# Kernel optimization log

Measured on AMD Instinct MI355X. Metric: run time of the kernel, lower is better.

The kernel has to match this reference:

```python
import jax, jax.numpy as jnp
import numpy as np

B, SEQ, D = 2, 1024, 768
E, H = 8, 3072          # num_experts, expert hidden (mlp_ratio=4)
CAPACITY = 2            # k = CAPACITY * num_tokens


def setup_inputs() -> dict:
    key = jax.random.key(0)
    ks = jax.random.split(key, 6)
    x = jax.random.normal(ks[0], (B, SEQ, D), dtype=jnp.float32)
    gate_weight = jax.random.normal(ks[1], (E, D), dtype=jnp.float32) * 0.006
    w1 = jax.random.normal(ks[2], (E, D, H), dtype=jnp.float32) * (1.0 / np.sqrt(D))
    b1 = jnp.zeros((E, H), dtype=jnp.float32)
    w2 = jax.random.normal(ks[3], (E, H, D), dtype=jnp.float32) * (1.0 / np.sqrt(H))
    b2 = jnp.zeros((E, D), dtype=jnp.float32)
    return {"x": x, "gate_weight": gate_weight, "w1": w1, "b1": b1, "w2": w2, "b2": b2}


def reference(x, gate_weight, w1, b1, w2, b2):
    Bb, s, d = x.shape
    xf = x.reshape(-1, d)                     # [S, D]
    S = xf.shape[0]
    k = S * CAPACITY
    logits = xf @ gate_weight.T               # [S, E]
    scores = jax.nn.softmax(logits, axis=-1).T  # [E, S]
    # flattened top-k over all (expert, token) pairs -> sparse gate matrix
    vals, idx = jax.lax.top_k(scores.reshape(-1), k)
    gate = jnp.zeros((E * S,), dtype=x.dtype).at[idx].add(vals).reshape(E, S)
    # expert MLPs (GELU-tanh) applied per expert; zero gate entries kill
    # non-routed (expert, token) pairs -> same math as gather/MLP/scatter.
    h = jax.nn.gelu(jnp.einsum('sd,edh->esh', xf, w1) + b1[:, None, :], approximate=True)
    out = jnp.einsum('esh,ehd->esd', h, w2) + b2[:, None, :]   # [E, S, D]
    y = jnp.einsum('es,esd->sd', gate, out)    # weighted combine + sum over experts
    return y.reshape(Bb, s, d)
```

## Files before the change

### kernel.cpp

```cpp
#include <hip/hip_runtime.h>
#include <math.h>

#define S_TOK 2048
#define NEXP  8
#define DDIM  768
#define HDIM  3072
#define KSEL  4096

typedef __attribute__((ext_vector_type(8))) short short8;
typedef __attribute__((ext_vector_type(4))) float f32x4;
typedef __attribute__((ext_vector_type(2))) unsigned int u32x2;

__device__ __forceinline__ unsigned short f2bf(float f) {
  unsigned u = __float_as_uint(f);
  u += 0x7fffu + ((u >> 16) & 1u);
  return (unsigned short)(u >> 16);
}

__device__ __forceinline__ float gelu_fast(float v) {
  float u = 0.7978845608028654f * (v + 0.044715f * v * v * v);
  float t = __expf(-2.0f * fabsf(u));
  float th = (1.0f - t) / (1.0f + t);
  th = copysignf(th, u);
  return 0.5f * v * (1.0f + th);
}

__global__ __launch_bounds__(256) void zero_kernel(float* __restrict__ p, int n) {
  int i = blockIdx.x * 256 + threadIdx.x;
  if (i < n) p[i] = 0.f;
}

__global__ __launch_bounds__(256) void convx_kernel(const float* __restrict__ x,
                                                    short* __restrict__ xb) {
  int i = (blockIdx.x * 256 + threadIdx.x) * 8;
  float4 a = *(const float4*)(x + i);
  float4 b = *(const float4*)(x + i + 4);
  short8 v;
  v[0] = (short)f2bf(a.x); v[1] = (short)f2bf(a.y);
  v[2] = (short)f2bf(a.z); v[3] = (short)f2bf(a.w);
  v[4] = (short)f2bf(b.x); v[5] = (short)f2bf(b.y);
  v[6] = (short)f2bf(b.z); v[7] = (short)f2bf(b.w);
  *(short8*)(xb + i) = v;
}

__global__ __launch_bounds__(256) void gate_kernel(
    const float* __restrict__ x, const float* __restrict__ gw,
    float* __restrict__ scores)
{
  int tid  = threadIdx.x;
  int lane = tid & 63;
  int wid  = tid >> 6;
  int token = blockIdx.x * 4 + wid;
  const float* xr = x + (size_t)token * DDIM;

  float acc[NEXP];
#pragma unroll
  for (int e = 0; e < NEXP; ++e) acc[e] = 0.f;

  for (int d = lane; d < DDIM; d += 64) {
    float xv = xr[d];
#pragma unroll
    for (int e = 0; e < NEXP; ++e) acc[e] += xv * gw[e * DDIM + d];
  }
#pragma unroll
  for (int e = 0; e < NEXP; ++e) {
    for (int off = 32; off; off >>= 1) acc[e] += __shfl_down(acc[e], off, 64);
  }
  if (lane == 0) {
    float m = acc[0];
#pragma unroll
    for (int e = 1; e < NEXP; ++e) m = fmaxf(m, acc[e]);
    float p[NEXP], s = 0.f;
#pragma unroll
    for (int e = 0; e < NEXP; ++e) { p[e] = expf(acc[e] - m); s += p[e]; }
    float inv = 1.0f / s;
#pragma unroll
    for (int e = 0; e < NEXP; ++e) scores[e * S_TOK + token] = p[e] * inv;
  }
}

__device__ unsigned block_scan_excl(unsigned v, volatile unsigned* wsum) {
  int tid = threadIdx.x, lane = tid & 63, wid = tid >> 6;
  __syncthreads();
  unsigned x = v;
#pragma unroll
  for (int off = 1; off < 64; off <<= 1) {
    unsigned t = __shfl_up(x, off, 64);
    if (lane >= off) x += t;
  }
  if (lane == 63) wsum[wid] = x;
  __syncthreads();
  if (tid < 64) {
    unsigned w = (lane < 16) ? wsum[lane] : 0u;
#pragma unroll
    for (int off = 1; off < 16; off <<= 1) {
      unsigned t = __shfl_up(w, off, 64);
      if (lane >= off) w += t;
    }
    if (lane < 16) wsum[lane] = w;
  }
  __syncthreads();
  unsigned woff = (wid > 0) ? wsum[wid - 1] : 0u;
  return woff + (x - v);
}

__global__ __launch_bounds__(1024) void select_kernel(
    const float* __restrict__ scores,
    int* __restrict__ tokenlist, float* __restrict__ slotgate,
    int* __restrict__ offsets)
{
  __shared__ unsigned cnt;
  __shared__ unsigned wsum[16];
  int tid = threadIdx.x;
  int base = tid * 16;

  float sv[16]; unsigned key[16];
#pragma unroll
  for (int j = 0; j < 16; ++j) {
    sv[j] = scores[base + j];
    key[j] = __float_as_uint(sv[j]);
  }

  unsigned lo = 0, hi = 0x3F800000u;
  while (lo < hi) {
    unsigned mid = lo + ((hi - lo + 1) >> 1);
    if (tid == 0) cnt = 0;
    __syncthreads();
    unsigned c = 0;
#pragma unroll
    for (int j = 0; j < 16; ++j) c += (key[j] >= mid) ? 1u : 0u;
    for (int off = 32; off; off >>= 1) c += __shfl_down(c, off, 64);
    if ((tid & 63) == 0) atomicAdd(&cnt, c);
    __syncthreads();
    unsigned tot = cnt;
    __syncthreads();
    if (tot >= (unsigned)KSEL) lo = mid; else hi = mid - 1;
  }
  unsigned V = lo;

  if (tid == 0) cnt = 0;
  __syncthreads();
  {
    unsigned c = 0;
#pragma unroll
    for (int j = 0; j < 16; ++j) c += (key[j] > V) ? 1u : 0u;
    for (int off = 32; off; off >>= 1) c += __shfl_down(c, off, 64);
    if ((tid & 63) == 0) atomicAdd(&cnt, c);
  }
  __syncthreads();
  int need = KSEL - (int)cnt;
  __syncthreads();

  unsigned tloc = 0;
#pragma unroll
  for (int j = 0; j < 16; ++j) tloc += (key[j] == V) ? 1u : 0u;
  unsigned texcl = block_scan_excl(tloc, wsum);

  unsigned selmask = 0, sloc = 0, trun = texcl;
#pragma unroll
  for (int j = 0; j < 16; ++j) {
    bool f;
    if (key[j] > V) f = true;
    else if (key[j] == V) { f = ((int)trun < need); ++trun; }
    else f = false;
    if (f) { selmask |= (1u << j); ++sloc; }
  }
  unsigned sexcl = block_scan_excl(sloc, wsum);

  if ((tid & 127) == 0) offsets[tid >> 7] = (int)sexcl;
  if (tid == 0) offsets[NEXP] = KSEL;

  unsigned p = sexcl;
#pragma unroll
  for (int j = 0; j < 16; ++j) {
    int i = base + j;
    if (selmask & (1u << j)) {
      tokenlist[p] = i & (S_TOK - 1);
      slotgate[p] = sv[j];
      ++p;
    }
  }
}

template <int MODE>
__global__ __launch_bounds__(256) void moe_mfma(
    const short* __restrict__ Abase, const float* __restrict__ W,
    const float* __restrict__ bias, void* __restrict__ outp,
    const int* __restrict__ offsets, const int* __restrict__ tokenlist,
    const float* __restrict__ slotgate)
{
  const int e = (int)blockIdx.x;
  const int K = (MODE == 1) ? DDIM : HDIM;
  const int N = (MODE == 1) ? HDIM : DDIM;
  const int tile  = (MODE == 1) ? (int)blockIdx.z : ((int)blockIdx.z >> 2);
  const int split = (MODE == 1) ? 0 : ((int)blockIdx.z & 3);
  const int klen  = 768;
  const int kb = split * klen;

  const int r0 = offsets[e];
  const int rows = offsets[e + 1] - r0;
  const int rowbase = tile << 7;
  if (rowbase >= rows) return;
  int vr = rows - rowbase; if (vr > 128) vr = 128;
  const int colbase = (int)blockIdx.y << 7;

  __shared__ short As0[128 * 40];
  __shared__ short As1[128 * 40];
  __shared__ __align__(16) short Bs0[32 * 128];
  __shared__ __align__(16) short Bs1[32 * 128];
  const unsigned bs0_lds = (unsigned)(uintptr_t)&Bs0[0];
  const unsigned bs1_lds = (unsigned)(uintptr_t)&Bs1[0];

  const int tid = threadIdx.x;
  const int lane = tid & 63;
  const int wid = tid >> 6;
  const int wr = (wid >> 1) << 6;
  const int wc = (wid & 1) << 6;
  const int l15 = lane & 15;
  const int lq = lane >> 4;

  const int ar = tid >> 1;
  const int ak = (tid & 1) << 4;
  const short* arow;
  {
    int cr = (ar < vr) ? ar : (vr - 1);
    if (MODE == 1) arow = Abase + (size_t)tokenlist[r0 + rowbase + cr] * DDIM;
    else           arow = Abase + (size_t)(r0 + rowbase + cr) * HDIM + kb;
  }

  const int sk = tid >> 3;
  const int g8 = tid & 7;
  const float* wsrc = W + (size_t)e * K * N + (size_t)kb * N + colbase + g8 * 16;
  const int bwoff = ((((sk >> 2) << 3) + g8) << 6) + ((sk & 3) << 4);

  f32x4 acc[4][4];
#pragma unroll
  for (int i = 0; i < 4; ++i)
#pragma unroll
    for (int j = 0; j < 4; ++j) acc[i][j] = (f32x4){0.f, 0.f, 0.f, 0.f};

  short8 avA0, avA1;
  float4 bw[4];

#define LOAD_AB(KN)                                              \
  {                                                              \
    avA0 = *(const short8*)(arow + (KN) + ak);                   \
    avA1 = *(const short8*)(arow + (KN) + ak + 8);               \
    const float* wp = wsrc + (size_t)((KN) + sk) * N;            \
    _Pragma("unroll")                                            \
    for (int q = 0; q < 4; ++q) bw[q] = *(const float4*)(wp + 4 * q); \
  }

#define WRITE_LDS(AS, BS)                                        \
  {                                                              \
    *(short8*)&AS[ar * 40 + ak] = avA0;                          \
    *(short8*)&AS[ar * 40 + ak + 8] = avA1;                      \
    _Pragma("unroll")                                            \
    for (int q = 0; q < 4; ++q) {                                \
      u32x2 pk;                                                  \
      pk[0] = (unsigned)f2bf(bw[q].x) | ((unsigned)f2bf(bw[q].y) << 16); \
      pk[1] = (unsigned)f2bf(bw[q].z) | ((unsigned)f2bf(bw[q].w) << 16); \
      *(u32x2*)((short*)BS + bwoff + 4 * q) = pk;                \
    }                                                            \
  }

#define KSTEP(RA, RBLDS, WA, WB, KC)                             \
  {                                                              \
    short8 af[4], bfr[4];                                        \
    _Pragma("unroll")                                            \
    for (int i = 0; i < 4; ++i)                                  \
      af[i] = *(const short8*)&RA[(wr + i * 16 + l15) * 40 + lq * 8]; \
    _Pragma("unroll")                                            \
    for (int j = 0; j < 4; ++j) {                                \
      unsigned off = (RBLDS) + ((unsigned)((lq << 4) + (wc >> 4) + j) << 7) + \
                     ((unsigned)l15 << 3);                       \
      union { short8 s; u32x2 u[2]; } fb;                        \
      asm volatile("ds_read_b64_tr_b16 %0, %2 offset:0\n\t"      \
                   "ds_read_b64_tr_b16 %1, %2 offset:1024"       \
                   : "=&v"(fb.u[0]), "=&v"(fb.u[1]) : "v"(off)); \
      bfr[j] = fb.s;                                             \
    }                                                            \
    if ((KC) + 32 < klen) {                                      \
      WRITE_LDS(WA, WB);                                         \
      if ((KC) + 64 < klen) LOAD_AB((KC) + 64);                  \
    }                                                            \
    asm volatile("s_waitcnt lgkmcnt(0)" ::: "memory");           \
    __builtin_amdgcn_sched_barrier(0);                           \
    _Pragma("unroll")                                            \
    for (int i = 0; i < 4; ++i)                                  \
      _Pragma("unroll")                                          \
      for (int j = 0; j < 4; ++j)                                \
        acc[i][j] = __builtin_amdgcn_mfma_f32_16x16x32_bf16(af[i], bfr[j], acc[i][j], 0, 0, 0); \
    __syncthreads();                                             \
  }

  LOAD_AB(0);
  WRITE_LDS(As0, Bs0);
  LOAD_AB(32);
  __syncthreads();

#pragma unroll 1
  for (int k0 = 0; k0 < klen; k0 += 64) {
    KSTEP(As0, bs0_lds, As1, Bs1, k0);
    KSTEP(As1, bs1_lds, As0, Bs0, k0 + 32);
  }

  if (MODE == 1) {
    short* hb = (short*)outp;
    const float* bp = bias + (size_t)e * N + colbase;
#pragma unroll
    for (int i = 0; i < 4; ++i) {
      int rb = wr + i * 16 + lq * 4;
#pragma unroll
      for (int j = 0; j < 4; ++j) {
        int col = wc + j * 16 + l15;
        float bvv = bp[col];
#pragma unroll
        for (int p = 0; p < 4; ++p) {
          int r = rb + p;
          if (r < vr)
            hb[(size_t)(r0 + rowbase + r) * HDIM + colbase + col] =
                (short)f2bf(gelu_fast(acc[i][j][p] + bvv));
        }
      }
    }
  } else {
    float* y = (float*)outp;
    const float* bp = bias + (size_t)e * N + colbase;
#pragma unroll
    for (int i = 0; i < 4; ++i) {
      int rb = wr + i * 16 + lq * 4;
#pragma unroll
      for (int p = 0; p < 4; ++p) {
        int r = rb + p;
        if (r < vr) {
          int gi = r0 + rowbase + r;
          float g = slotgate[gi];
          float* yrow = y + (size_t)tokenlist[gi] * N + colbase;
#pragma unroll
          for (int j = 0; j < 4; ++j) {
            int col = wc + j * 16 + l15;
            float v = acc[i][j][p] + (split == 0 ? bp[col] : 0.f);
            atomicAdd(&yrow[col], g * v);
          }
        }
      }
    }
  }
}

extern "C" void kernel_launch(void* const* d_in, const int* in_sizes, int n_in,
                              void* d_out, int out_size, void* d_ws, size_t ws_size,
                              hipStream_t stream) {
  const float* x  = (const float*)d_in[0];
  const float* gw = (const float*)d_in[1];
  const float* w1 = (const float*)d_in[2];
  const float* b1 = (const float*)d_in[3];
  const float* w2 = (const float*)d_in[4];
  const float* b2 = (const float*)d_in[5];
  float* y = (float*)d_out;

  char* ws = (char*)d_ws;
  float* scores    = (float*)(ws);
  int*   tokenlist = (int*)(ws + (64 << 10));
  float* slotgate  = (float*)(ws + (80 << 10));
  int*   offsets   = (int*)(ws + (96 << 10));
  short* xbf       = (short*)(ws + (128 << 10));
  short* hbuf      = (short*)(ws + (128 << 10) + (size_t)S_TOK * DDIM * 2);

  zero_kernel<<<(out_size + 255) / 256, 256, 0, stream>>>(y, out_size);
  convx_kernel<<<S_TOK * DDIM / 2048, 256, 0, stream>>>(x, xbf);
  gate_kernel<<<S_TOK / 4, 256, 0, stream>>>(x, gw, scores);
  select_kernel<<<1, 1024, 0, stream>>>(scores, tokenlist, slotgate, offsets);

  dim3 g1(NEXP, HDIM / 128, 16);
  moe_mfma<1><<<g1, 256, 0, stream>>>(xbf, w1, b1, hbuf, offsets, tokenlist, slotgate);
  dim3 g2(NEXP, DDIM / 128, 64);
  moe_mfma<2><<<g2, 256, 0, stream>>>(hbuf, w2, b2, y, offsets, tokenlist, slotgate);
}
```

Measured before the change: 210.4 us.

## Shrink expert GEMM tiles to 128x64 with 2 waves and single-buffered LDS

The expert MLP GEMM kernel moves from 256-thread blocks computing 128x128 tiles to 128-thread blocks computing 128x64 tiles, which doubles the grid along the output columns. LDS double buffering is dropped: each k-step now does sync, write, sync, then loads the next tile and computes. The aim is more resident blocks and smaller LDS per block for better occupancy. In exchange, the A tile is re-read by twice as many blocks, there are two barriers per k-step, and LDS writes no longer overlap compute.

Result: slower. 238.4 us (+13.3%).

```diff
diff --git a/kernel.cpp b/kernel.cpp
--- a/kernel.cpp
+++ b/kernel.cpp
@@ -183,7 +183,7 @@
 }
 
 template <int MODE>
-__global__ __launch_bounds__(256) void moe_mfma(
+__global__ __launch_bounds__(128) void moe_mfma(
     const short* __restrict__ Abase, const float* __restrict__ W,
     const float* __restrict__ bias, void* __restrict__ outp,
     const int* __restrict__ offsets, const int* __restrict__ tokenlist,
@@ -202,36 +202,30 @@
   const int rowbase = tile << 7;
   if (rowbase >= rows) return;
   int vr = rows - rowbase; if (vr > 128) vr = 128;
-  const int colbase = (int)blockIdx.y << 7;
-
-  __shared__ short As0[128 * 40];
-  __shared__ short As1[128 * 40];
-  __shared__ __align__(16) short Bs0[32 * 128];
-  __shared__ __align__(16) short Bs1[32 * 128];
-  const unsigned bs0_lds = (unsigned)(uintptr_t)&Bs0[0];
-  const unsigned bs1_lds = (unsigned)(uintptr_t)&Bs1[0];
+  const int colbase = (int)blockIdx.y << 6;
+
+  __shared__ short As[128 * 40];
+  __shared__ __align__(16) short Bs[32 * 64];
+  const unsigned bs_lds = (unsigned)(uintptr_t)&Bs[0];
 
   const int tid = threadIdx.x;
   const int lane = tid & 63;
   const int wid = tid >> 6;
-  const int wr = (wid >> 1) << 6;
-  const int wc = (wid & 1) << 6;
+  const int wr = wid << 6;
   const int l15 = lane & 15;
   const int lq = lane >> 4;
 
-  const int ar = tid >> 1;
-  const int ak = (tid & 1) << 4;
   const short* arow;
   {
-    int cr = (ar < vr) ? ar : (vr - 1);
+    int cr = (tid < vr) ? tid : (vr - 1);
     if (MODE == 1) arow = Abase + (size_t)tokenlist[r0 + rowbase + cr] * DDIM;
     else           arow = Abase + (size_t)(r0 + rowbase + cr) * HDIM + kb;
   }
 
-  const int sk = tid >> 3;
-  const int g8 = tid & 7;
-  const float* wsrc = W + (size_t)e * K * N + (size_t)kb * N + colbase + g8 * 16;
-  const int bwoff = ((((sk >> 2) << 3) + g8) << 6) + ((sk & 3) << 4);
+  const int brow = tid >> 2;
+  const int bc4 = tid & 3;
+  const float* wsrc = W + (size_t)e * K * N + (size_t)kb * N + colbase + bc4 * 4;
+  const int bwbase = ((tid >> 4) << 9) + ((brow & 3) << 5) + (bc4 << 3);
 
   f32x4 acc[4][4];
 #pragma unroll
@@ -239,70 +233,61 @@
 #pragma unroll
     for (int j = 0; j < 4; ++j) acc[i][j] = (f32x4){0.f, 0.f, 0.f, 0.f};
 
-  short8 avA0, avA1;
+  short8 av[4];
   float4 bw[4];
 
 #define LOAD_AB(KN)                                              \
   {                                                              \
-    avA0 = *(const short8*)(arow + (KN) + ak);                   \
-    avA1 = *(const short8*)(arow + (KN) + ak + 8);               \
-    const float* wp = wsrc + (size_t)((KN) + sk) * N;            \
     _Pragma("unroll")                                            \
-    for (int q = 0; q < 4; ++q) bw[q] = *(const float4*)(wp + 4 * q); \
-  }
-
-#define WRITE_LDS(AS, BS)                                        \
+    for (int m = 0; m < 4; ++m)                                  \
+      av[m] = *(const short8*)(arow + (KN) + m * 8);             \
+    const float* wp = wsrc + (size_t)((KN) + brow) * N;          \
+    _Pragma("unroll")                                            \
+    for (int q = 0; q < 4; ++q) bw[q] = *(const float4*)(wp + q * 16); \
+  }
+
+#define WRITE_LDS()                                              \
   {                                                              \
-    *(short8*)&AS[ar * 40 + ak] = avA0;                          \
-    *(short8*)&AS[ar * 40 + ak + 8] = avA1;                      \
+    _Pragma("unroll")                                            \
+    for (int m = 0; m < 4; ++m)                                  \
+      *(short8*)&As[tid * 40 + m * 8] = av[m];                   \
     _Pragma("unroll")                                            \
     for (int q = 0; q < 4; ++q) {                                \
       u32x2 pk;                                                  \
       pk[0] = (unsigned)f2bf(bw[q].x) | ((unsigned)f2bf(bw[q].y) << 16); \
       pk[1] = (unsigned)f2bf(bw[q].z) | ((unsigned)f2bf(bw[q].w) << 16); \
-      *(u32x2*)((short*)BS + bwoff + 4 * q) = pk;                \
+      *(u32x2*)((char*)Bs + bwbase + (q << 7)) = pk;             \
     }                                                            \
   }
 
-#define KSTEP(RA, RBLDS, WA, WB, KC)                             \
-  {                                                              \
-    short8 af[4], bfr[4];                                        \
-    _Pragma("unroll")                                            \
-    for (int i = 0; i < 4; ++i)                                  \
-      af[i] = *(const short8*)&RA[(wr + i * 16 + l15) * 40 + lq * 8]; \
-    _Pragma("unroll")                                            \
-    for (int j = 0; j < 4; ++j) {                                \
-      unsigned off = (RBLDS) + ((unsigned)((lq << 4) + (wc >> 4) + j) << 7) + \
-                     ((unsigned)l15 << 3);                       \
-      union { short8 s; u32x2 u[2]; } fb;                        \
-      asm volatile("ds_read_b64_tr_b16 %0, %2 offset:0\n\t"      \
-                   "ds_read_b64_tr_b16 %1, %2 offset:1024"       \
-                   : "=&v"(fb.u[0]), "=&v"(fb.u[1]) : "v"(off)); \
-      bfr[j] = fb.s;                                             \
-    }                                                            \
-    if ((KC) + 32 < klen) {                                      \
-      WRITE_LDS(WA, WB);                                         \
-      if ((KC) + 64 < klen) LOAD_AB((KC) + 64);                  \
-    }                                                            \
-    asm volatile("s_waitcnt lgkmcnt(0)" ::: "memory");           \
-    __builtin_amdgcn_sched_barrier(0);                           \
-    _Pragma("unroll")                                            \
-    for (int i = 0; i < 4; ++i)                                  \
-      _Pragma("unroll")                                          \
-      for (int j = 0; j < 4; ++j)                                \
-        acc[i][j] = __builtin_amdgcn_mfma_f32_16x16x32_bf16(af[i], bfr[j], acc[i][j], 0, 0, 0); \
-    __syncthreads();                                             \
-  }
-
   LOAD_AB(0);
-  WRITE_LDS(As0, Bs0);
-  LOAD_AB(32);
-  __syncthreads();
 
 #pragma unroll 1
-  for (int k0 = 0; k0 < klen; k0 += 64) {
-    KSTEP(As0, bs0_lds, As1, Bs1, k0);
-    KSTEP(As1, bs1_lds, As0, Bs0, k0 + 32);
+  for (int k0 = 0; k0 < klen; k0 += 32) {
+    __syncthreads();
+    WRITE_LDS();
+    __syncthreads();
+    if (k0 + 32 < klen) LOAD_AB(k0 + 32);
+    short8 af[4], bfr[4];
+#pragma unroll
+    for (int i = 0; i < 4; ++i)
+      af[i] = *(const short8*)&As[(wr + i * 16 + l15) * 40 + lq * 8];
+#pragma unroll
+    for (int j = 0; j < 4; ++j) {
+      unsigned off = bs_lds + ((unsigned)(8 * lq + j) << 7) + ((unsigned)l15 << 3);
+      union { short8 s; u32x2 u[2]; } fb;
+      asm volatile("ds_read_b64_tr_b16 %0, %2 offset:0\n\t"
+                   "ds_read_b64_tr_b16 %1, %2 offset:512"
+                   : "=&v"(fb.u[0]), "=&v"(fb.u[1]) : "v"(off));
+      bfr[j] = fb.s;
+    }
+    asm volatile("s_waitcnt lgkmcnt(0)" ::: "memory");
+    __builtin_amdgcn_sched_barrier(0);
+#pragma unroll
+    for (int i = 0; i < 4; ++i)
+#pragma unroll
+      for (int j = 0; j < 4; ++j)
+        acc[i][j] = __builtin_amdgcn_mfma_f32_16x16x32_bf16(af[i], bfr[j], acc[i][j], 0, 0, 0);
   }
 
   if (MODE == 1) {
@@ -313,7 +298,7 @@
       int rb = wr + i * 16 + lq * 4;
 #pragma unroll
       for (int j = 0; j < 4; ++j) {
-        int col = wc + j * 16 + l15;
+        int col = j * 16 + l15;
         float bvv = bp[col];
 #pragma unroll
         for (int p = 0; p < 4; ++p) {
@@ -339,7 +324,7 @@
           float* yrow = y + (size_t)tokenlist[gi] * N + colbase;
 #pragma unroll
           for (int j = 0; j < 4; ++j) {
-            int col = wc + j * 16 + l15;
+            int col = j * 16 + l15;
             float v = acc[i][j][p] + (split == 0 ? bp[col] : 0.f);
             atomicAdd(&yrow[col], g * v);
           }
@@ -373,8 +358,8 @@
   gate_kernel<<<S_TOK / 4, 256, 0, stream>>>(x, gw, scores);
   select_kernel<<<1, 1024, 0, stream>>>(scores, tokenlist, slotgate, offsets);
 
-  dim3 g1(NEXP, HDIM / 128, 16);
-  moe_mfma<1><<<g1, 256, 0, stream>>>(xbf, w1, b1, hbuf, offsets, tokenlist, slotgate);
-  dim3 g2(NEXP, DDIM / 128, 64);
-  moe_mfma<2><<<g2, 256, 0, stream>>>(hbuf, w2, b2, y, offsets, tokenlist, slotgate);
-}
+  dim3 g1(NEXP, HDIM / 64, 16);
+  moe_mfma<1><<<g1, 128, 0, stream>>>(xbf, w1, b1, hbuf, offsets, tokenlist, slotgate);
+  dim3 g2(NEXP, DDIM / 64, 64);
+  moe_mfma<2><<<g2, 128, 0, stream>>>(hbuf, w2, b2, y, offsets, tokenlist, slotgate);
+}
```
